# Kernel optimization log

Hardware: AMD Instinct MI355X
Metric: run time of the kernel (lower is better)

Reference implementation:

```python
import jax, jax.numpy as jnp
import numpy as np

B, N, L, K, CD, H, DH, D = 2, 2048, 1024, 16, 2, 4, 128, 128
HD = H * DH  # 512
FQ = 2.0  # embedding_freq_multiplier for query-invariant embedding
FV = 2.0  # embedding_freq_multiplier for value-invariant embedding
SCALE = 1.0 / float(np.sqrt(DH))


def _ln(x, s, b, eps=1e-6):
    m = x.mean(-1, keepdims=True)
    v = x.var(-1, keepdims=True)
    return (x - m) / jnp.sqrt(v + eps) * s + b


def _ffn(x, w1, b1, ls, lb, w2, b2):
    # PointwiseFFN: Dense -> gelu -> LayerNorm -> Dense
    h = jax.nn.gelu(x @ w1 + b1)
    return _ln(h, ls, lb) @ w2 + b2


def _rff(inv, Bm, freq, w1, b1, w2, b2):
    # random-Fourier-feature embedding of the invariant, then 2-layer MLP
    proj = (2.0 * jnp.pi * freq) * (inv @ Bm)          # (..., DH//2)
    feats = jnp.concatenate([jnp.sin(proj), jnp.cos(proj)], axis=-1)  # (..., DH)
    return jax.nn.gelu(feats @ w1 + b1) @ w2 + b2      # (..., DH)


def _forward(x, p, c, window_sigma, x_h,
             rffq, rffv,
             eq_w1, eq_b1, eq_w2, eq_b2,
             ev_w1, ev_b1, ev_w2, ev_b2,
             wq, bq, wk, bk, wv, bv,
             cw1, cb1, cls, clb, cw2, cb2,
             ivw1, ivb1, ivls, ivlb, ivw2, ivb2,
             mw1, mb1, mls, mlb, mw2, mb2,
             wo, bo):
    # relative-position invariant: (B, N, L, CD)
    rel = x[:, :, None, :] - p[:, None, :, :]
    dist = jnp.linalg.norm(rel, axis=-1)                         # (B, N, L)
    nearest = jnp.argsort(dist, axis=-1)[:, :, :K]               # (B, N, K)
    inv = jnp.take_along_axis(
        rel, jnp.broadcast_to(nearest[..., None], nearest.shape + (CD,)), axis=2)  # (B,N,K,CD)
    cg = jnp.take_along_axis(c[:, None, :, :], nearest[..., None], axis=2)         # (B,N,K,D)

    q = _rff(inv, rffq, FQ, eq_w1, eq_b1, eq_w2, eq_b2) @ wq + bq  # (B,N,K,HD)
    k_ = cg @ wk + bk                                              # (B,N,K,HD)
    v = cg @ wv + bv                                               # (B,N,K,HD)

    # conditioned value transform
    inv_emb_v = _rff(inv, rffv, FV, ev_w1, ev_b1, ev_w2, ev_b2)    # (B,N,K,DH)
    gb = _ffn(x_h, cw1, cb1, cls, clb, cw2, cb2)                   # (B,N,2*DH)
    g, bt = jnp.split(gb, 2, axis=-1)
    inv_emb_v = inv_emb_v * (1 + g[:, :, None, :]) + bt[:, :, None, :]
    vgb = _ffn(inv_emb_v, ivw1, ivb1, ivls, ivlb, ivw2, ivb2)      # (B,N,K,2*HD)
    vg, vb = jnp.split(vgb, 2, axis=-1)
    v = v * (1 + vg) + vb
    v = v.reshape(v.shape[:-1] + (H, DH))                          # (B,N,K,H,DH)
    v = _ffn(v, mw1, mb1, mls, mlb, mw2, mb2)

    q = q.reshape(q.shape[:-1] + (H, DH))
    k_ = k_.reshape(k_.shape[:-1] + (H, DH))
    att = (q * k_).sum(axis=-1) * SCALE                            # (B,N,K,H)

    # gaussian window in log-space, gathered at nearest latents
    gw_full = -0.5 * (dist ** 2)[..., None] / (window_sigma[:, None, :, :] ** 2)  # (B,N,L,1)
    gw = jnp.take_along_axis(gw_full, nearest[..., None], axis=2)                  # (B,N,K,1)
    att = jax.nn.softmax(att + gw, axis=-2)                        # softmax over K

    y = (att[..., None] * v).sum(axis=2)                           # (B,N,H,DH)
    y = y.reshape(y.shape[0], y.shape[1], HD)
    return y @ wo + bo                                             # (B,N,DH)


def setup_inputs() -> dict:
    key = jax.random.key(0)
    ks = jax.random.split(key, 24)
    dn = lambda k, i, o: jax.random.normal(k, (i, o), jnp.float32) / float(np.sqrt(i))
    z = lambda n: jnp.zeros((n,), jnp.float32)
    o = lambda n: jnp.ones((n,), jnp.float32)
    inp = {
        'x': jax.random.uniform(ks[0], (B, N, CD), jnp.float32),
        'p': jax.random.uniform(ks[1], (B, L, CD), jnp.float32),
        'c': jax.random.normal(ks[2], (B, L, D), jnp.float32),
        'window_sigma': jax.random.uniform(ks[3], (B, L, 1), jnp.float32, minval=0.1, maxval=0.5),
        'x_h': jax.random.normal(ks[4], (B, N, DH), jnp.float32),
        'rffq': jax.random.normal(ks[5], (CD, DH // 2), jnp.float32),
        'rffv': jax.random.normal(ks[6], (CD, DH // 2), jnp.float32),
        'eq_w1': dn(ks[7], DH, DH), 'eq_b1': z(DH),
        'eq_w2': dn(ks[8], DH, DH), 'eq_b2': z(DH),
        'ev_w1': dn(ks[9], DH, DH), 'ev_b1': z(DH),
        'ev_w2': dn(ks[10], DH, DH), 'ev_b2': z(DH),
        'wq': dn(ks[11], DH, HD), 'bq': z(HD),
        'wk': dn(ks[12], D, HD), 'bk': z(HD),
        'wv': dn(ks[13], D, HD), 'bv': z(HD),
        'cw1': dn(ks[14], DH, DH), 'cb1': z(DH), 'cls': o(DH), 'clb': z(DH),
        'cw2': dn(ks[15], DH, 2 * DH), 'cb2': z(2 * DH),
        'ivw1': dn(ks[16], DH, DH), 'ivb1': z(DH), 'ivls': o(DH), 'ivlb': z(DH),
        'ivw2': dn(ks[17], DH, 2 * HD), 'ivb2': z(2 * HD),
        'mw1': dn(ks[18], DH, DH), 'mb1': z(DH), 'mls': o(DH), 'mlb': z(DH),
        'mw2': dn(ks[19], DH, DH), 'mb2': z(DH),
        'wo': dn(ks[20], HD, DH), 'bo': z(DH),
    }
    return inp


def reference(x, p, c, window_sigma, x_h,
              rffq, rffv,
              eq_w1, eq_b1, eq_w2, eq_b2,
              ev_w1, ev_b1, ev_w2, ev_b2,
              wq, bq, wk, bk, wv, bv,
              cw1, cb1, cls, clb, cw2, cb2,
              ivw1, ivb1, ivls, ivlb, ivw2, ivb2,
              mw1, mb1, mls, mlb, mw2, mb2,
              wo, bo):
    return _forward(x, p, c, window_sigma, x_h,
                    rffq, rffv,
                    eq_w1, eq_b1, eq_w2, eq_b2,
                    ev_w1, ev_b1, ev_w2, ev_b2,
                    wq, bq, wk, bk, wv, bv,
                    cw1, cb1, cls, clb, cw2, cb2,
                    ivw1, ivb1, ivls, ivlb, ivw2, ivb2,
                    mw1, mb1, mls, mlb, mw2, mb2,
                    wo, bo)
```

## Files before the change

kernel.cpp:

```cpp
#include <hip/hip_runtime.h>
#include <hip/hip_bf16.h>
#include <math.h>

#define Bx  2
#define Nx  2048
#define Lx  1024
#define Kx  16
#define Hx  4
#define DHx 128
#define HDx 512
#define NROW 65536

typedef unsigned short u16;
typedef unsigned int   u32;
typedef unsigned long long u64;

#define ALD 132
#define KLD 520
#define LDW 136

typedef __attribute__((ext_vector_type(8))) short bf16x8;
typedef __attribute__((ext_vector_type(4))) float f32x4;
typedef __attribute__((ext_vector_type(4))) unsigned int u32x4;

__device__ __forceinline__ float bf(u16 v) { return __uint_as_float(((u32)v) << 16); }

__device__ __forceinline__ u16 f2bf(float f) {
  u32 u = __float_as_uint(f);
  u32 r = (u + 0x7fffu + ((u >> 16) & 1u)) >> 16;
  return (u16)r;
}

__device__ __forceinline__ void split2(float v, u16* h, u16* l) {
  u16 hh = f2bf(v);
  *h = hh;
  *l = f2bf(v - bf(hh));
}

__device__ __forceinline__ bf16x8 ntload8(const u16* p) {
  u32x4 v = __builtin_nontemporal_load((const u32x4*)p);
  bf16x8 r;
  *(u32x4*)&r = v;
  return r;
}

template <int ISB>
__device__ __forceinline__ float ldg1(const void* p, int i) {
  if (ISB) return bf(((const u16*)p)[i]);
  return ((const float*)p)[i];
}
template <int ISB>
__device__ __forceinline__ void ldg2(const void* p, int i, float& a, float& b) {
  if (ISB) {
    u32 u = *(const u32*)((const u16*)p + i);
    a = __uint_as_float(u << 16); b = __uint_as_float(u & 0xffff0000u);
  } else {
    float2 v = *(const float2*)((const float*)p + i);
    a = v.x; b = v.y;
  }
}
template <int ISB>
__device__ __forceinline__ void ldg4(const void* p, int i, float* o) {
  if (ISB) {
    uint2 u = *(const uint2*)((const u16*)p + i);
    o[0] = __uint_as_float(u.x << 16); o[1] = __uint_as_float(u.x & 0xffff0000u);
    o[2] = __uint_as_float(u.y << 16); o[3] = __uint_as_float(u.y & 0xffff0000u);
  } else {
    float4 v = *(const float4*)((const float*)p + i);
    o[0] = v.x; o[1] = v.y; o[2] = v.z; o[3] = v.w;
  }
}
template <int ISB>
__device__ __forceinline__ void ldg8(const void* p, int i, float* o) {
  if (ISB) {
    uint4 u = *(const uint4*)((const u16*)p + i);
    o[0] = __uint_as_float(u.x << 16); o[1] = __uint_as_float(u.x & 0xffff0000u);
// ... 495 lines not shown
    for (int r = 0; r < 16; r++) s += sm.ATT[r * 4 + h] * sm.KV[r * KLD + j];
    sm.YV[j] = s;
  }
  __syncthreads();

  if (t < 128) {
    float s = ldg1<ISB>(bo, t);
    for (int j = 0; j < 512; j++) s += sm.YV[j] * ldg1<ISB>(wo, j * 128 + t);
    stg1<ISB>(outp, bid * 128 + t, s);
  }
}


#define OFF_WQ    0
#define OFF_WK    65536
#define OFF_WV    131072
#define OFF_IVW2  196608
#define OFF_EQW1  327680
#define OFF_EQW2  344064
#define OFF_EVW1  360448
#define OFF_EVW2  376832
#define OFF_IVW1  393216
#define OFF_MW1   409600
#define OFF_MW2   425984
#define OFF_CW1   442368
#define OFF_CW2   458752
#define OFF_WO    491520
#define WT_TOTAL  557056

__device__ __attribute__((aligned(16))) u16 g_wth[WT_TOTAL];
__device__ __attribute__((aligned(16))) u16 g_wtl[WT_TOTAL];

__device__ __attribute__((aligned(16))) u16 gAh[NROW * 128], gAl[NROW * 128];
__device__ __attribute__((aligned(16))) u16 gBh[4096 * 128], gBl[4096 * 128];
__device__ __attribute__((aligned(16))) u16 gCGh[NROW * 128], gCGl[NROW * 128];
__device__ __attribute__((aligned(16))) u16 gVHh[NROW * 128], gVHl[NROW * 128];
__device__ __attribute__((aligned(16))) u16 gEIh[NROW * 128], gEIl[NROW * 128];
__device__ float gY[4096 * 512];
__device__ float gGVBT[4096 * 256];
__device__ float gATT[4096 * 64];
__device__ float gINVS[4096 * 32];
__device__ float gGWS[4096 * 16];
__device__ int   gIDX[NROW];

__global__ void k_prep32(
    const void* wq, const void* wk, const void* wv, const void* ivw2,
    const void* eqw1, const void* eqw2, const void* evw1, const void* evw2,
    const void* ivw1, const void* mw1, const void* mw2,
    const void* cw1, const void* cw2, const void* wo,
    const int* __restrict__ flag) {
  if (*flag != 0) return;
  int gid = blockIdx.x * 256 + threadIdx.x;
  float w;
  if (gid >= OFF_WO) {
    int local = gid - OFF_WO;
    int n = local >> 9, k = local & 511;
    w = ((const float*)wo)[k * 128 + n];
  } else {
    const float* src; int N; int local;
    if      (gid < OFF_WK)   { src = (const float*)wq;   N = 512;  local = gid - OFF_WQ; }
    else if (gid < OFF_WV)   { src = (const float*)wk;   N = 512;  local = gid - OFF_WK; }
    else if (gid < OFF_IVW2) { src = (const float*)wv;   N = 512;  local = gid - OFF_WV; }
    else if (gid < OFF_EQW1) { src = (const float*)ivw2; N = 1024; local = gid - OFF_IVW2; }
    else if (gid < OFF_EQW2) { src = (const float*)eqw1; N = 128;  local = gid - OFF_EQW1; }
    else if (gid < OFF_EVW1) { src = (const float*)eqw2; N = 128;  local = gid - OFF_EQW2; }
    else if (gid < OFF_EVW2) { src = (const float*)evw1; N = 128;  local = gid - OFF_EVW1; }
    else if (gid < OFF_IVW1) { src = (const float*)evw2; N = 128;  local = gid - OFF_EVW2; }
    else if (gid < OFF_MW1)  { src = (const float*)ivw1; N = 128;  local = gid - OFF_IVW1; }
    else if (gid < OFF_MW2)  { src = (const float*)mw1;  N = 128;  local = gid - OFF_MW1; }
    else if (gid < OFF_CW1)  { src = (const float*)mw2;  N = 128;  local = gid - OFF_MW2; }
    else if (gid < OFF_CW2)  { src = (const float*)cw1;  N = 128;  local = gid - OFF_CW1; }
    else                     { src = (const float*)cw2;  N = 256;  local = gid - OFF_CW2; }
    int n = local >> 7, k = local & 127;
    w = src[k * N + n];
  }
  u16 h = f2bf(w);
  g_wth[gid] = h;
  g_wtl[gid] = f2bf(w - bf(h));
}

__device__ __forceinline__ f32x4 mfma16(bf16x8 a, bf16x8 b, f32x4 c) {
  return __builtin_amdgcn_mfma_f32_16x16x32_bf16(a, b, c, 0, 0, 0);
}

__device__ __forceinline__ void stageW(
    const u16* __restrict__ wth, const u16* __restrict__ wtl, int srcStride,
    u16* __restrict__ sWh, u16* __restrict__ sWl, int t) {
#pragma unroll
  for (int it = 0; it < 4; it++) {
    int i = t + it * 512;
    int row = i >> 4, c8 = (i & 15) * 8;
    *(uint4*)(sWh + row * LDW + c8) = *(const uint4*)(wth + (size_t)row * srcStride + c8);
    *(uint4*)(sWl + row * LDW + c8) = *(const uint4*)(wtl + (size_t)row * srcStride + c8);
  }
}

__device__ __forceinline__ void loadA(
    const u16* __restrict__ Ah, const u16* __restrict__ Al, size_t abase,
    int lane, bf16x8 ah[4], bf16x8 al[4]) {
  int r = lane & 15, kg = lane >> 4;
#pragma unroll
  for (int kc = 0; kc < 4; kc++) {
    ah[kc] = *(const bf16x8*)(Ah + abase + (size_t)r * 128 + kc * 32 + kg * 8);
    al[kc] = *(const bf16x8*)(Al + abase + (size_t)r * 128 + kc * 32 + kg * 8);
  }
}

__device__ __forceinline__ void loadA_nt(
    const u16* __restrict__ Ah, const u16* __restrict__ Al, size_t abase,
    int lane, bf16x8 ah[4], bf16x8 al[4]) {
  int r = lane & 15, kg = lane >> 4;
#pragma unroll
  for (int kc = 0; kc < 4; kc++) {
    ah[kc] = ntload8(Ah + abase + (size_t)r * 128 + kc * 32 + kg * 8);
    al[kc] = ntload8(Al + abase + (size_t)r * 128 + kc * 32 + kg * 8);
  }
}

__device__ __forceinline__ void loadA_lds(
    const u16* __restrict__ sAh_w, const u16* __restrict__ sAl_w,
    int lane, bf16x8 ah[4], bf16x8 al[4]) {
  int r = lane & 15, kg = lane >> 4;
#pragma unroll
  for (int kc = 0; kc < 4; kc++) {
    ah[kc] = *(const bf16x8*)(sAh_w + r * LDW + kc * 32 + kg * 8);
    al[kc] = *(const bf16x8*)(sAl_w + r * LDW + kc * 32 + kg * 8);
  }
}

__device__ __forceinline__ void core16L(
    const bf16x8 ah[4], const bf16x8 al[4],
    const u16* __restrict__ sWh, const u16* __restrict__ sWl,
    f32x4 acc[8], int lane) {
  int r = lane & 15, kg = lane >> 4;
#pragma unroll
  for (int tile = 0; tile < 8; tile++) {
    int cc = tile * 16 + r;
    f32x4 a = {0.f, 0.f, 0.f, 0.f};
#pragma unroll
    for (int kc = 0; kc < 4; kc++) {
      bf16x8 bh = *(const bf16x8*)(sWh + cc * LDW + kc * 32 + kg * 8);
      bf16x8 bl = *(const bf16x8*)(sWl + cc * LDW + kc * 32 + kg * 8);
      a = mfma16(ah[kc], bh, a);
      a = mfma16(ah[kc], bl, a);
      a = mfma16(al[kc], bh, a);
    }
    acc[tile] = a;
  }
}

__device__ __forceinline__ void storeACT(
    f32x4 acc[8], const float* __restrict__ bias, int act,
    u16* __restrict__ sAh_w, u16* __restrict__ sAl_w, int lane) {
  int r = lane & 15, kg = lane >> 4;
#pragma unroll
  for (int tile = 0; tile < 8; tile++) {
    int cc = tile * 16 + r;
    float bc = bias[cc];
#pragma unroll
    for (int q = 0; q < 4; q++) {
      float v = acc[tile][q] + bc;
      if (act) v = geluf(v);
      int o = (kg * 4 + q) * LDW + cc;
      split2(v, sAh_w + o, sAl_w + o);
    }
  }
}

__device__ __forceinline__ void storeACT_ln(
    f32x4 acc[8], const float* __restrict__ bias,
    const float* __restrict__ sc, const float* __restrict__ bi,
    u16* __restrict__ sAh_w, u16* __restrict__ sAl_w, int lane) {
  int r = lane & 15, kg = lane >> 4;
  float v[8][4];
  float s[4] = {0.f, 0.f, 0.f, 0.f}, s2[4] = {0.f, 0.f, 0.f, 0.f};
#pragma unroll
  for (int tile = 0; tile < 8; tile++) {
    float bc = bias[tile * 16 + r];
#pragma unroll
    for (int q = 0; q < 4; q++) {
      float x = geluf(acc[tile][q] + bc);
      v[tile][q] = x; s[q] += x; s2[q] += x * x;
    }
  }
#pragma unroll
  for (int m = 1; m <= 8; m <<= 1) {
#pragma unroll
    for (int q = 0; q < 4; q++) {
      s[q]  += __shfl_xor(s[q], m);
      s2[q] += __shfl_xor(s2[q], m);
    }
  }
  float mean[4], rstd[4];
#pragma unroll
  for (int q = 0; q < 4; q++) {
// ... 55 lines not shown
    }
  }
}


__global__ __launch_bounds__(256) void k_topk(
    const float* __restrict__ x, const float* __restrict__ p,
    const float* __restrict__ sig, const int* __restrict__ flag) {
  if (*flag != 0) return;
  int t = threadIdx.x, lane = t & 63, w = t >> 6;
  int n = blockIdx.x * 4 + w, b = n >> 11;
  float qx = x[n * 2 + 0], qy = x[n * 2 + 1];
  u64 keys[16];
#pragma unroll
  for (int e = 0; e < 16; e++) {
    int l = e * 64 + lane;
    float px = p[(b * Lx + l) * 2 + 0];
    float py = p[(b * Lx + l) * 2 + 1];
    float dx = qx - px, dy = qy - py;
    float d2 = __fadd_rn(__fmul_rn(dx, dx), __fmul_rn(dy, dy));
    keys[e] = (((u64)__float_as_uint(__fsqrt_rn(d2))) << 32) | (u32)l;
  }
#pragma unroll 1
  for (int kk = 0; kk < Kx; kk++) {
    u64 kmin = keys[0];
#pragma unroll
    for (int e = 1; e < 16; e++) kmin = kmin < keys[e] ? kmin : keys[e];
#pragma unroll
    for (int m = 1; m <= 32; m <<= 1) {
      u64 o = shfl_xor_u64(kmin, m);
      kmin = kmin < o ? kmin : o;
    }
    if (lane == 0) {
      int l = (int)(kmin & 0xffffffffu);
      float d = __uint_as_float((u32)(kmin >> 32));
      float px = p[(b * Lx + l) * 2 + 0];
      float py = p[(b * Lx + l) * 2 + 1];
      float sg = sig[b * Lx + l];
      gIDX[n * 16 + kk] = l;
      gINVS[n * 32 + kk * 2 + 0] = qx - px;
      gINVS[n * 32 + kk * 2 + 1] = qy - py;
      gGWS[n * 16 + kk] = (-0.5f * (d * d)) / (sg * sg);
    }
#pragma unroll
    for (int e = 0; e < 16; e++) if (keys[e] == kmin) keys[e] = ~0ull;
  }
}

__global__ __launch_bounds__(512, 1) void k_c1(
    const float* __restrict__ xh, const float* __restrict__ cb1,
    const float* __restrict__ cls, const float* __restrict__ clb,
    const int* __restrict__ flag) {
  if (*flag != 0) return;
  __shared__ u16 sWh[128 * LDW], sWl[128 * LDW];
  int t = threadIdx.x, lane = t & 63, w = t >> 6;
  stageW(g_wth + OFF_CW1, g_wtl + OFF_CW1, 128, sWh, sWl, t);
  size_t rb = (size_t)blockIdx.x * 128 + w * 16;
  int r = lane & 15, kg = lane >> 4;
  bf16x8 ah[4], al[4];
#pragma unroll
  for (int kc = 0; kc < 4; kc++) {
    const float* src = xh + (rb + r) * 128 + kc * 32 + kg * 8;
#pragma unroll
    for (int e = 0; e < 8; e++) {
      float xv = src[e];
      u16 hh = f2bf(xv);
      ah[kc][e] = (short)hh;
      al[kc][e] = (short)f2bf(xv - bf(hh));
    }
  }
  __syncthreads();
  f32x4 acc[8];
  core16L(ah, al, sWh, sWl, acc, lane);
  store16_gelu_ln(acc, cb1, cls, clb, gBh, gBl, rb * 128, lane);
}

__global__ __launch_bounds__(512, 1) void k_c2(
    const float* __restrict__ cb2, const int* __restrict__ flag) {
  if (*flag != 0) return;
  __shared__ u16 sWh[128 * LDW], sWl[128 * LDW];
  int t = threadIdx.x, lane = t & 63, w = t >> 6;
  size_t rb = (size_t)blockIdx.x * 128 + w * 16;
  int r = lane & 15, kg = lane >> 4;
  bf16x8 ah[4], al[4];
  loadA(gBh, gBl, rb * 128, lane, ah, al);
#pragma unroll 1
  for (int half = 0; half < 2; half++) {
    stageW(g_wth + OFF_CW2 + half * 128 * 128,
           g_wtl + OFF_CW2 + half * 128 * 128, 128, sWh, sWl, t);
    __syncthreads();
    f32x4 acc[8];
    core16L(ah, al, sWh, sWl, acc, lane);
#pragma unroll
    for (int tile = 0; tile < 8; tile++) {
      int cc = half * 128 + tile * 16 + r;
      float bc = cb2[cc];
#pragma unroll
      for (int q = 0; q < 4; q++)
        gGVBT[(rb + kg * 4 + q) * 256 + cc] = acc[tile][q] + bc;
    }
    __syncthreads();
  }
}

__global__ __launch_bounds__(512) void k_gather(
    const float* __restrict__ c, const float* __restrict__ rffq,
    const float* __restrict__ rffv, const int* __restrict__ flag) {
  if (*flag != 0) return;
  int t = threadIdx.x;
  size_t row = (size_t)blockIdx.x * 64 + (t >> 3);
  int cbase = (t & 7) * 16;
  int n = (int)(row >> 4), b = n >> 11;
  int li = gIDX[row];
  const float* cp = c + ((size_t)(b * Lx + li)) * 128 + cbase;
  float ix = gINVS[n * 32 + (row & 15) * 2 + 0];
  float iy = gINVS[n * 32 + (row & 15) * 2 + 1];
  size_t o = row * 128 + cbase;
#pragma unroll
  for (int half = 0; half < 2; half++) {
    float4 va = ((const float4*)cp)[half * 2 + 0];
    float4 vb = ((const float4*)cp)[half * 2 + 1];
    float cv[8] = {va.x, va.y, va.z, va.w, vb.x, vb.y, vb.z, vb.w};
    bf16x8 ch_, cl_, qh_, ql_, eh_, el_;
#pragma unroll
    for (int j = 0; j < 8; j++) {
      int col = cbase + half * 8 + j, cc = col & 63;
      u16 hh = f2bf(cv[j]);
      ch_[j] = (short)hh; cl_[j] = (short)f2bf(cv[j] - bf(hh));
      float pq = 12.566370614359172f * (ix * rffq[cc] + iy * rffq[64 + cc]);
      float pv = 12.566370614359172f * (ix * rffv[cc] + iy * rffv[64 + cc]);
      float vq = (col < 64) ? sinf(pq) : cosf(pq);
      float vv = (col < 64) ? sinf(pv) : cosf(pv);
      u16 qh16 = f2bf(vq);
      qh_[j] = (short)qh16; ql_[j] = (short)f2bf(vq - bf(qh16));
      u16 eh16 = f2bf(vv);
      eh_[j] = (short)eh16; el_[j] = (short)f2bf(vv - bf(eh16));
    }
    *(bf16x8*)(gCGh + o + half * 8) = ch_;
    *(bf16x8*)(gCGl + o + half * 8) = cl_;
    *(bf16x8*)(gAh  + o + half * 8) = qh_;
    *(bf16x8*)(gAl  + o + half * 8) = ql_;
    *(bf16x8*)(gVHh + o + half * 8) = eh_;
    *(bf16x8*)(gVHl + o + half * 8) = el_;
  }
}

__global__ __launch_bounds__(512, 1) void k_qatt(
    const float* __restrict__ eqb1, const float* __restrict__ eqb2,
    const float* __restrict__ bq, const float* __restrict__ bk,
    const int* __restrict__ flag) {
  if (*flag != 0) return;
  __shared__ u16 sWh[128 * LDW], sWl[128 * LDW];
  __shared__ u16 sAh[128 * LDW], sAl[128 * LDW];
  int t = threadIdx.x, lane = t & 63, w = t >> 6;
  size_t rb = (size_t)blockIdx.x * 128 + w * 16;
  u16* myAh = sAh + (w * 16) * LDW;
  u16* myAl = sAl + (w * 16) * LDW;
  int r = lane & 15, kg = lane >> 4;
  stageW(g_wth + OFF_EQW1, g_wtl + OFF_EQW1, 128, sWh, sWl, t);
  bf16x8 ah[4], al[4];
  loadA_nt(gAh, gAl, rb * 128, lane, ah, al);
  __syncthreads();
  f32x4 acc[8];
  core16L(ah, al, sWh, sWl, acc, lane);
  storeACT(acc, eqb1, 1, myAh, myAl, lane);
  __syncthreads();
  stageW(g_wth + OFF_EQW2, g_wtl + OFF_EQW2, 128, sWh, sWl, t);
  __syncthreads();
  loadA_lds(myAh, myAl, lane, ah, al);
  core16L(ah, al, sWh, sWl, acc, lane);
  storeACT(acc, eqb2, 0, myAh, myAl, lane);
  bf16x8 qfh[4], qfl[4], ckh[4], ckl[4];
  loadA_lds(myAh, myAl, lane, qfh, qfl);
  loadA_nt(gCGh, gCGl, rb * 128, lane, ckh, ckl);
  int pt = blockIdx.x * 8 + w;
#pragma unroll 1
  for (int h = 0; h < 4; h++) {
    __syncthreads();
    stageW(g_wth + OFF_WQ + h * 16384, g_wtl + OFF_WQ + h * 16384, 128, sWh, sWl, t);
    __syncthreads();
    f32x4 dq[8];
    core16L(qfh, qfl, sWh, sWl, dq, lane);
    __syncthreads();
    stageW(g_wth + OFF_WK + h * 16384, g_wtl + OFF_WK + h * 16384, 128, sWh, sWl, t);
    __syncthreads();
    float pr[4] = {0.f, 0.f, 0.f, 0.f};
#pragma unroll
    for (int tile = 0; tile < 8; tile++) {
      int cc = tile * 16 + r;
      f32x4 dk = {0.f, 0.f, 0.f, 0.f};
#pragma unroll
      for (int kc = 0; kc < 4; kc++) {
        bf16x8 bh = *(const bf16x8*)(sWh + cc * LDW + kc * 32 + kg * 8);
        bf16x8 bl = *(const bf16x8*)(sWl + cc * LDW + kc * 32 + kg * 8);
        dk = mfma16(ckh[kc], bh, dk);
        dk = mfma16(ckh[kc], bl, dk);
        dk = mfma16(ckl[kc], bh, dk);
      }
      float bqv = bq[h * 128 + cc], bkv = bk[h * 128 + cc];
#pragma unroll
      for (int q = 0; q < 4; q++)
        pr[q] += (dq[tile][q] + bqv) * (dk[q] + bkv);
    }
#pragma unroll
    for (int m = 1; m <= 8; m <<= 1) {
#pragma unroll
      for (int q = 0; q < 4; q++) pr[q] += __shfl_xor(pr[q], m);
    }
    if (r == 0) {
#pragma unroll
      for (int q = 0; q < 4; q++)
        gATT[pt * 64 + h * 16 + kg * 4 + q] = pr[q] * 0.08838834764831845f;
    }
  }
}

__global__ __launch_bounds__(256) void k_soft(const int* __restrict__ flag) {
  if (*flag != 0) return;
  int id = blockIdx.x * 256 + threadIdx.x;
  int pt = id >> 2, h = id & 3;
  float mx = -1e30f;
  for (int k = 0; k < 16; k++) {
    float v = gATT[pt * 64 + h * 16 + k] + gGWS[pt * 16 + k];
    mx = fmaxf(mx, v);
  }
  float ssum = 0.0f;
  float ev[16];
  for (int k = 0; k < 16; k++) {
    float e = expf(gATT[pt * 64 + h * 16 + k] + gGWS[pt * 16 + k] - mx);
    ev[k] = e; ssum += e;
  }
  float inv = 1.0f / fmaxf(ssum, 1e-37f);
  for (int k = 0; k < 16; k++) gATT[pt * 64 + h * 16 + k] = ev[k] * inv;
}

__global__ __launch_bounds__(512, 1) void k_echain(
    const float* __restrict__ evb1, const float* __restrict__ evb2,
    const float* __restrict__ ivb1, const float* __restrict__ ivls,
    const float* __restrict__ ivlb, const int* __restrict__ flag) {
  if (*flag != 0) return;
  __shared__ u16 sWh[128 * LDW], sWl[128 * LDW];
  __shared__ u16 sAh[128 * LDW], sAl[128 * LDW];
  int t = threadIdx.x, lane = t & 63, w = t >> 6;
  size_t rb = (size_t)blockIdx.x * 128 + w * 16;
  u16* myAh = sAh + (w * 16) * LDW;
  u16* myAl = sAl + (w * 16) * LDW;
  int r = lane & 15, kg = lane >> 4;
  int pt = blockIdx.x * 8 + w;
  stageW(g_wth + OFF_EVW1, g_wtl + OFF_EVW1, 128, sWh, sWl, t);
  bf16x8 ah[4], al[4];
  loadA_nt(gVHh, gVHl, rb * 128, lane, ah, al);
  __syncthreads();
  f32x4 acc[8];
  core16L(ah, al, sWh, sWl, acc, lane);
  storeACT(acc, evb1, 1, myAh, myAl, lane);
  __syncthreads();
  stageW(g_wth + OFF_EVW2, g_wtl + OFF_EVW2, 128, sWh, sWl, t);
  __syncthreads();
  loadA_lds(myAh, myAl, lane, ah, al);
  core16L(ah, al, sWh, sWl, acc, lane);
#pragma unroll
  for (int tile = 0; tile < 8; tile++) {
    int cc = tile * 16 + r;
    float bc = evb2[cc];
    float gv = gGVBT[pt * 256 + cc];
    float bt = gGVBT[pt * 256 + 128 + cc];
#pragma unroll
    for (int q = 0; q < 4; q++) {
      float v = (acc[tile][q] + bc) * (1.0f + gv) + bt;
      int o = (kg * 4 + q) * LDW + cc;
      split2(v, myAh + o, myAl + o);
    }
  }
  __syncthreads();
  stageW(g_wth + OFF_IVW1, g_wtl + OFF_IVW1, 128, sWh, sWl, t);
  __syncthreads();
  loadA_lds(myAh, myAl, lane, ah, al);
  core16L(ah, al, sWh, sWl, acc, lane);
  store16_gelu_ln(acc, ivb1, ivls, ivlb, gEIh, gEIl, rb * 128, lane);
}

__global__ __launch_bounds__(512, 1) void k_vchain(
    const float* __restrict__ bv, const float* __restrict__ ivb2,
    const float* __restrict__ mb1, const float* __restrict__ mls,
    const float* __restrict__ mlb, const float* __restrict__ mb2,
    const int* __restrict__ flag) {
  if (*flag != 0) return;
  __shared__ u16 sWh[128 * LDW], sWl[128 * LDW];
  __shared__ u16 sAh[128 * LDW], sAl[128 * LDW];
  int t = threadIdx.x, lane = t & 63, w = t >> 6;
  size_t rb = (size_t)blockIdx.x * 128 + w * 16;
  u16* myAh = sAh + (w * 16) * LDW;
  u16* myAl = sAl + (w * 16) * LDW;
  int r = lane & 15, kg = lane >> 4;
  int pt = blockIdx.x * 8 + w;
#pragma unroll 1
  for (int h = 0; h < 4; h++) {
    f32x4 vv[8];
    __syncthreads();
    stageW(g_wth + OFF_WV + (size_t)(h * 128) * 128,
           g_wtl + OFF_WV + (size_t)(h * 128) * 128, 128, sWh, sWl, t);
    {
      bf16x8 ckh[4], ckl[4];
      loadA_nt(gCGh, gCGl, rb * 128, lane, ckh, ckl);
      __syncthreads();
      core16L(ckh, ckl, sWh, sWl, vv, lane);
    }
    f32x4 ag[8];
    __syncthreads();
    stageW(g_wth + OFF_IVW2 + (size_t)(h * 128) * 128,
           g_wtl + OFF_IVW2 + (size_t)(h * 128) * 128, 128, sWh, sWl, t);
    {
      bf16x8 eih[4], eil[4];
      loadA_nt(gEIh, gEIl, rb * 128, lane, eih, eil);
      __syncthreads();
      core16L(eih, eil, sWh, sWl, ag, lane);
    }
    __syncthreads();
    stageW(g_wth + OFF_IVW2 + (size_t)(512 + h * 128) * 128,
           g_wtl + OFF_IVW2 + (size_t)(512 + h * 128) * 128, 128, sWh, sWl, t);
    {
      bf16x8 eih[4], eil[4];
      loadA_nt(gEIh, gEIl, rb * 128, lane, eih, eil);
      __syncthreads();
#pragma unroll
      for (int tile = 0; tile < 8; tile++) {
        int cc = tile * 16 + r;
        f32x4 ab = {0.f, 0.f, 0.f, 0.f};
#pragma unroll
        for (int kc = 0; kc < 4; kc++) {
          bf16x8 bh = *(const bf16x8*)(sWh + cc * LDW + kc * 32 + kg * 8);
          bf16x8 bl = *(const bf16x8*)(sWl + cc * LDW + kc * 32 + kg * 8);
          ab = mfma16(eih[kc], bh, ab);
          ab = mfma16(eih[kc], bl, ab);
          ab = mfma16(eil[kc], bh, ab);
        }
        float bvv = bv[h * 128 + cc];
        float bgv = ivb2[h * 128 + cc], bbv = ivb2[512 + h * 128 + cc];
#pragma unroll
        for (int q = 0; q < 4; q++) {
          float x = vv[tile][q] + bvv;
          u16 hh = f2bf(x);
          u16 ll = f2bf(x - bf(hh));
          float v = bf(hh) + bf(ll);
          float nv = v * (1.f + (ag[tile][q] + bgv)) + (ab[q] + bbv);
          int o = (kg * 4 + q) * LDW + cc;
          split2(nv, myAh + o, myAl + o);
        }
      }
    }
    __syncthreads();
    stageW(g_wth + OFF_MW1, g_wtl + OFF_MW1, 128, sWh, sWl, t);
    __syncthreads();
    {
      bf16x8 vh_[4], vl_[4];
      loadA_lds(myAh, myAl, lane, vh_, vl_);
      f32x4 acc[8];
      core16L(vh_, vl_, sWh, sWl, acc, lane);
      storeACT_ln(acc, mb1, mls, mlb, myAh, myAl, lane);
    }
    __syncthreads();
    stageW(g_wth + OFF_MW2, g_wtl + OFF_MW2, 128, sWh, sWl, t);
    __syncthreads();
    {
      bf16x8 vh_[4], vl_[4];
      loadA_lds(myAh, myAl, lane, vh_, vl_);
      f32x4 acc[8];
      core16L(vh_, vl_, sWh, sWl, acc, lane);
      float attv[4];
#pragma unroll
      for (int q = 0; q < 4; q++) attv[q] = gATT[pt * 64 + h * 16 + kg * 4 + q];
#pragma unroll
      for (int tile = 0; tile < 8; tile++) {
        int cc = tile * 16 + r;
        float mb = mb2[cc];
        float s = 0.f;
#pragma unroll
        for (int q = 0; q < 4; q++) s += attv[q] * (acc[tile][q] + mb);
        s += __shfl_xor(s, 16);
        s += __shfl_xor(s, 32);
        if (kg == 0) gY[(size_t)pt * 512 + h * 128 + cc] = s;
      }
    }
  }
}

__global__ __launch_bounds__(512, 1) void k_out(
    const float* __restrict__ bo, const int* __restrict__ flag,
    float* __restrict__ outp) {
  if (*flag != 0) return;
  __shared__ u16 sWh[128 * LDW], sWl[128 * LDW];
  int t = threadIdx.x, lane = t & 63, w = t >> 6;
  size_t rb = (size_t)blockIdx.x * 128 + w * 16;
  int r = lane & 15, kg = lane >> 4;
  f32x4 acc[8] = {};
#pragma unroll 1
  for (int kb = 0; kb < 4; kb++) {
    stageW(g_wth + OFF_WO + kb * 128, g_wtl + OFF_WO + kb * 128, 512, sWh, sWl, t);
    bf16x8 ah[4], al[4];
#pragma unroll
    for (int kc = 0; kc < 4; kc++) {
      const float* src = gY + (rb + r) * 512 + kb * 128 + kc * 32 + kg * 8;
#pragma unroll
      for (int e = 0; e < 8; e++) {
        float xv = src[e];
        u16 hh = f2bf(xv);
        ah[kc][e] = (short)hh;
        al[kc][e] = (short)f2bf(xv - bf(hh));
      }
    }
    __syncthreads();
#pragma unroll
    for (int tile = 0; tile < 8; tile++) {
      int cc = tile * 16 + r;
      f32x4 a = acc[tile];
#pragma unroll
      for (int kc = 0; kc < 4; kc++) {
        bf16x8 bh = *(const bf16x8*)(sWh + cc * LDW + kc * 32 + kg * 8);
        bf16x8 bl = *(const bf16x8*)(sWl + cc * LDW + kc * 32 + kg * 8);
        a = mfma16(ah[kc], bh, a);
        a = mfma16(ah[kc], bl, a);
        a = mfma16(al[kc], bh, a);
      }
      acc[tile] = a;
    }
    __syncthreads();
  }
#pragma unroll
  for (int tile = 0; tile < 8; tile++) {
    int cc = tile * 16 + r;
    float bc = bo[cc];
#pragma unroll
    for (int q = 0; q < 4; q++)
      outp[(rb + kg * 4 + q) * 128 + cc] = acc[tile][q] + bc;
  }
}

extern "C" void kernel_launch(void* const* d_in, const int* in_sizes, int n_in,
                              void* d_out, int out_size, void* d_ws, size_t ws_size,
                              hipStream_t stream) {
  (void)in_sizes; (void)n_in; (void)out_size; (void)ws_size;
  int* flag = (int*)d_ws;

  k_sniff<<<1, 64, 0, stream>>>(d_in[23], flag);

  k_prep32<<<WT_TOTAL / 256, 256, 0, stream>>>(
      d_in[15], d_in[17], d_in[19], d_in[31],
      d_in[7], d_in[9], d_in[11], d_in[13],
      d_in[27], d_in[33], d_in[37],
      d_in[21], d_in[25], d_in[39], flag);

  k_topk<<<1024, 256, 0, stream>>>((const float*)d_in[0], (const float*)d_in[1],
                                   (const float*)d_in[3], flag);
  k_c1<<<32, 512, 0, stream>>>((const float*)d_in[4], (const float*)d_in[22],
                               (const float*)d_in[23], (const float*)d_in[24], flag);
  k_c2<<<32, 512, 0, stream>>>((const float*)d_in[26], flag);
  k_gather<<<1024, 512, 0, stream>>>((const float*)d_in[2], (const float*)d_in[5],
                                     (const float*)d_in[6], flag);
  k_qatt<<<512, 512, 0, stream>>>((const float*)d_in[8], (const float*)d_in[10],
                                  (const float*)d_in[16], (const float*)d_in[18], flag);
  k_soft<<<64, 256, 0, stream>>>(flag);
  k_echain<<<512, 512, 0, stream>>>((const float*)d_in[12], (const float*)d_in[14],
                                    (const float*)d_in[28], (const float*)d_in[29],
                                    (const float*)d_in[30], flag);
  k_vchain<<<512, 512, 0, stream>>>((const float*)d_in[20], (const float*)d_in[32],
                                    (const float*)d_in[34], (const float*)d_in[35],
                                    (const float*)d_in[36], (const float*)d_in[38], flag);
  k_out<<<32, 512, 0, stream>>>((const float*)d_in[40], flag, (float*)d_out);

  k_fused<1><<<Bx * Nx, 256, 0, stream>>>(
      d_in[0], d_in[1], d_in[2], d_in[3], d_in[4], d_in[5], d_in[6],
      d_in[7], d_in[8], d_in[9], d_in[10],
// ... 8 lines not shown
```

Before: 732.0 us.

## Stage weights via global_load_lds DMA with XOR-swizzled layout and half-tile overlap

Weights are pre-swizzled in the prep kernel with an XOR pattern so they can be copied into unpadded 128x128 LDS tiles with direct global-to-LDS loads instead of register round-trips. Each weight tile is staged in two halves so the second half's load overlaps MFMA work on the first, and several redundant barriers are dropped. The intent is to cut LDS staging latency and bank conflicts. It relies on careful barrier placement around async LDS writes, which risks races if the ordering is wrong.

Result: slower. 781.7 us (+6.8%).

```diff
diff --git a/kernel.cpp b/kernel.cpp
--- a/kernel.cpp
+++ b/kernel.cpp
@@ -22,6 +22,9 @@
 typedef __attribute__((ext_vector_type(8))) short bf16x8;
 typedef __attribute__((ext_vector_type(4))) float f32x4;
 typedef __attribute__((ext_vector_type(4))) unsigned int u32x4;
+
+typedef const __attribute__((address_space(1))) void* as1_cvp;
+typedef __attribute__((address_space(3))) void* as3_vp;
 
 __device__ __forceinline__ float bf(u16 v) { return __uint_as_float(((u32)v) << 16); }
 
@@ -623,46 +626,75 @@
   if (*flag != 0) return;
   int gid = blockIdx.x * 256 + threadIdx.x;
   float w;
+  int dest;
   if (gid >= OFF_WO) {
     int local = gid - OFF_WO;
     int n = local >> 9, k = local & 511;
     w = ((const float*)wo)[k * 128 + n];
+    int cs = ((k >> 3) & 15) ^ (n & 15);
+    dest = OFF_WO + n * 512 + (k & 384) + (cs << 3) + (k & 7);
   } else {
-    const float* src; int N; int local;
-    if      (gid < OFF_WK)   { src = (const float*)wq;   N = 512;  local = gid - OFF_WQ; }
-    else if (gid < OFF_WV)   { src = (const float*)wk;   N = 512;  local = gid - OFF_WK; }
-    else if (gid < OFF_IVW2) { src = (const float*)wv;   N = 512;  local = gid - OFF_WV; }
-    else if (gid < OFF_EQW1) { src = (const float*)ivw2; N = 1024; local = gid - OFF_IVW2; }
-    else if (gid < OFF_EQW2) { src = (const float*)eqw1; N = 128;  local = gid - OFF_EQW1; }
-    else if (gid < OFF_EVW1) { src = (const float*)eqw2; N = 128;  local = gid - OFF_EQW2; }
-    else if (gid < OFF_EVW2) { src = (const float*)evw1; N = 128;  local = gid - OFF_EVW1; }
-    else if (gid < OFF_IVW1) { src = (const float*)evw2; N = 128;  local = gid - OFF_EVW2; }
-    else if (gid < OFF_MW1)  { src = (const float*)ivw1; N = 128;  local = gid - OFF_IVW1; }
-    else if (gid < OFF_MW2)  { src = (const float*)mw1;  N = 128;  local = gid - OFF_MW1; }
-    else if (gid < OFF_CW1)  { src = (const float*)mw2;  N = 128;  local = gid - OFF_MW2; }
-    else if (gid < OFF_CW2)  { src = (const float*)cw1;  N = 128;  local = gid - OFF_CW1; }
-    else                     { src = (const float*)cw2;  N = 256;  local = gid - OFF_CW2; }
+    const float* src; int N; int local; int base;
+    if      (gid < OFF_WK)   { src = (const float*)wq;   N = 512;  local = gid - OFF_WQ;   base = OFF_WQ; }
+    else if (gid < OFF_WV)   { src = (const float*)wk;   N = 512;  local = gid - OFF_WK;   base = OFF_WK; }
+    else if (gid < OFF_IVW2) { src = (const float*)wv;   N = 512;  local = gid - OFF_WV;   base = OFF_WV; }
+    else if (gid < OFF_EQW1) { src = (const float*)ivw2; N = 1024; local = gid - OFF_IVW2; base = OFF_IVW2; }
+    else if (gid < OFF_EQW2) { src = (const float*)eqw1; N = 128;  local = gid - OFF_EQW1; base = OFF_EQW1; }
+    else if (gid < OFF_EVW1) { src = (const float*)eqw2; N = 128;  local = gid - OFF_EQW2; base = OFF_EQW2; }
+    else if (gid < OFF_EVW2) { src = (const float*)evw1; N = 128;  local = gid - OFF_EVW1; base = OFF_EVW1; }
+    else if (gid < OFF_IVW1) { src = (const float*)evw2; N = 128;  local = gid - OFF_EVW2; base = OFF_EVW2; }
+    else if (gid < OFF_MW1)  { src = (const float*)ivw1; N = 128;  local = gid - OFF_IVW1; base = OFF_IVW1; }
+    else if (gid < OFF_MW2)  { src = (const float*)mw1;  N = 128;  local = gid - OFF_MW1;  base = OFF_MW1; }
+    else if (gid < OFF_CW1)  { src = (const float*)mw2;  N = 128;  local = gid - OFF_MW2;  base = OFF_MW2; }
+    else if (gid < OFF_CW2)  { src = (const float*)cw1;  N = 128;  local = gid - OFF_CW1;  base = OFF_CW1; }
+    else                     { src = (const float*)cw2;  N = 256;  local = gid - OFF_CW2;  base = OFF_CW2; }
     int n = local >> 7, k = local & 127;
     w = src[k * N + n];
+    int cs = (k >> 3) ^ (n & 15);
+    dest = base + n * 128 + (cs << 3) + (k & 7);
   }
   u16 h = f2bf(w);
-  g_wth[gid] = h;
-  g_wtl[gid] = f2bf(w - bf(h));
+  g_wth[dest] = h;
+  g_wtl[dest] = f2bf(w - bf(h));
 }
 
 __device__ __forceinline__ f32x4 mfma16(bf16x8 a, bf16x8 b, f32x4 c) {
   return __builtin_amdgcn_mfma_f32_16x16x32_bf16(a, b, c, 0, 0, 0);
 }
 
-__device__ __forceinline__ void stageW(
+__device__ __forceinline__ const bf16x8* wp(const u16* sW, int cc, int kc, int kg) {
+  return (const bf16x8*)(sW + cc * 128 + (((kc * 4 + kg) ^ (cc & 15)) << 3));
+}
+
+__device__ __forceinline__ void gll16(const u16* g, u16* l) {
+  __builtin_amdgcn_global_load_lds((as1_cvp)(const void*)g, (as3_vp)(void*)l, 16, 0, 0);
+}
+
+__device__ __forceinline__ void stageDMA(
     const u16* __restrict__ wth, const u16* __restrict__ wtl, int srcStride,
-    u16* __restrict__ sWh, u16* __restrict__ sWl, int t) {
+    u16* sWh, u16* sWl, int t) {
+  int w6 = t >> 6, lane = t & 63;
 #pragma unroll
   for (int it = 0; it < 4; it++) {
-    int i = t + it * 512;
-    int row = i >> 4, c8 = (i & 15) * 8;
-    *(uint4*)(sWh + row * LDW + c8) = *(const uint4*)(wth + (size_t)row * srcStride + c8);
-    *(uint4*)(sWl + row * LDW + c8) = *(const uint4*)(wtl + (size_t)row * srcStride + c8);
+    int seg = it * 8 + w6;
+    int chunk = seg * 64 + lane;
+    int row = chunk >> 4, cs = chunk & 15;
+    gll16(wth + (size_t)row * srcStride + cs * 8, sWh + (size_t)seg * 512);
+    gll16(wtl + (size_t)row * srcStride + cs * 8, sWl + (size_t)seg * 512);
+  }
+}
+
+__device__ __forceinline__ void stageH(
+    const u16* __restrict__ wth, const u16* __restrict__ wtl,
+    u16* sWh, u16* sWl, int t, int half) {
+  int w6 = t >> 6, lane = t & 63;
+#pragma unroll
+  for (int it = 0; it < 2; it++) {
+    int seg = half * 16 + it * 8 + w6;
+    int chunk = seg * 64 + lane;
+    int row = chunk >> 4, cs = chunk & 15;
+    gll16(wth + (size_t)row * 128 + cs * 8, sWh + (size_t)seg * 512);
+    gll16(wtl + (size_t)row * 128 + cs * 8, sWl + (size_t)seg * 512);
   }
 }
 
@@ -699,19 +731,20 @@
   }
 }
 
-__device__ __forceinline__ void core16L(
+template <int T0, int T1>
+__device__ __forceinline__ void core16L_r(
     const bf16x8 ah[4], const bf16x8 al[4],
     const u16* __restrict__ sWh, const u16* __restrict__ sWl,
     f32x4 acc[8], int lane) {
   int r = lane & 15, kg = lane >> 4;
 #pragma unroll
-  for (int tile = 0; tile < 8; tile++) {
+  for (int tile = T0; tile < T1; tile++) {
     int cc = tile * 16 + r;
     f32x4 a = {0.f, 0.f, 0.f, 0.f};
 #pragma unroll
     for (int kc = 0; kc < 4; kc++) {
-      bf16x8 bh = *(const bf16x8*)(sWh + cc * LDW + kc * 32 + kg * 8);
-      bf16x8 bl = *(const bf16x8*)(sWl + cc * LDW + kc * 32 + kg * 8);
+      bf16x8 bh = *wp(sWh, cc, kc, kg);
+      bf16x8 bl = *wp(sWl, cc, kc, kg);
       a = mfma16(ah[kc], bh, a);
       a = mfma16(ah[kc], bl, a);
       a = mfma16(al[kc], bh, a);
@@ -873,9 +906,9 @@
     const float* __restrict__ cls, const float* __restrict__ clb,
     const int* __restrict__ flag) {
   if (*flag != 0) return;
-  __shared__ u16 sWh[128 * LDW], sWl[128 * LDW];
+  __shared__ u16 sWh[128 * 128], sWl[128 * 128];
   int t = threadIdx.x, lane = t & 63, w = t >> 6;
-  stageW(g_wth + OFF_CW1, g_wtl + OFF_CW1, 128, sWh, sWl, t);
+  stageDMA(g_wth + OFF_CW1, g_wtl + OFF_CW1, 128, sWh, sWl, t);
   size_t rb = (size_t)blockIdx.x * 128 + w * 16;
   int r = lane & 15, kg = lane >> 4;
   bf16x8 ah[4], al[4];
@@ -892,14 +925,14 @@
   }
   __syncthreads();
   f32x4 acc[8];
-  core16L(ah, al, sWh, sWl, acc, lane);
+  core16L_r<0, 8>(ah, al, sWh, sWl, acc, lane);
   store16_gelu_ln(acc, cb1, cls, clb, gBh, gBl, rb * 128, lane);
 }
 
 __global__ __launch_bounds__(512, 1) void k_c2(
     const float* __restrict__ cb2, const int* __restrict__ flag) {
   if (*flag != 0) return;
-  __shared__ u16 sWh[128 * LDW], sWl[128 * LDW];
+  __shared__ u16 sWh[128 * 128], sWl[128 * 128];
   int t = threadIdx.x, lane = t & 63, w = t >> 6;
   size_t rb = (size_t)blockIdx.x * 128 + w * 16;
   int r = lane & 15, kg = lane >> 4;
@@ -907,11 +940,11 @@
   loadA(gBh, gBl, rb * 128, lane, ah, al);
 #pragma unroll 1
   for (int half = 0; half < 2; half++) {
-    stageW(g_wth + OFF_CW2 + half * 128 * 128,
-           g_wtl + OFF_CW2 + half * 128 * 128, 128, sWh, sWl, t);
+    stageDMA(g_wth + OFF_CW2 + half * 128 * 128,
+             g_wtl + OFF_CW2 + half * 128 * 128, 128, sWh, sWl, t);
     __syncthreads();
     f32x4 acc[8];
-    core16L(ah, al, sWh, sWl, acc, lane);
+    core16L_r<0, 8>(ah, al, sWh, sWl, acc, lane);
 #pragma unroll
     for (int tile = 0; tile < 8; tile++) {
       int cc = half * 128 + tile * 16 + r;
@@ -971,25 +1004,30 @@
     const float* __restrict__ bq, const float* __restrict__ bk,
     const int* __restrict__ flag) {
   if (*flag != 0) return;
-  __shared__ u16 sWh[128 * LDW], sWl[128 * LDW];
+  __shared__ u16 sWh[128 * 128], sWl[128 * 128];
   __shared__ u16 sAh[128 * LDW], sAl[128 * LDW];
   int t = threadIdx.x, lane = t & 63, w = t >> 6;
   size_t rb = (size_t)blockIdx.x * 128 + w * 16;
   u16* myAh = sAh + (w * 16) * LDW;
   u16* myAl = sAl + (w * 16) * LDW;
   int r = lane & 15, kg = lane >> 4;
-  stageW(g_wth + OFF_EQW1, g_wtl + OFF_EQW1, 128, sWh, sWl, t);
+  stageH(g_wth + OFF_EQW1, g_wtl + OFF_EQW1, sWh, sWl, t, 0);
   bf16x8 ah[4], al[4];
   loadA_nt(gAh, gAl, rb * 128, lane, ah, al);
   __syncthreads();
+  stageH(g_wth + OFF_EQW1, g_wtl + OFF_EQW1, sWh, sWl, t, 1);
   f32x4 acc[8];
-  core16L(ah, al, sWh, sWl, acc, lane);
+  core16L_r<0, 4>(ah, al, sWh, sWl, acc, lane);
+  __syncthreads();
+  core16L_r<4, 8>(ah, al, sWh, sWl, acc, lane);
   storeACT(acc, eqb1, 1, myAh, myAl, lane);
-  __syncthreads();
-  stageW(g_wth + OFF_EQW2, g_wtl + OFF_EQW2, 128, sWh, sWl, t);
-  __syncthreads();
+  stageH(g_wth + OFF_EQW2, g_wtl + OFF_EQW2, sWh, sWl, t, 0);
+  __syncthreads();
+  stageH(g_wth + OFF_EQW2, g_wtl + OFF_EQW2, sWh, sWl, t, 1);
   loadA_lds(myAh, myAl, lane, ah, al);
-  core16L(ah, al, sWh, sWl, acc, lane);
+  core16L_r<0, 4>(ah, al, sWh, sWl, acc, lane);
+  __syncthreads();
+  core16L_r<4, 8>(ah, al, sWh, sWl, acc, lane);
   storeACT(acc, eqb2, 0, myAh, myAl, lane);
   bf16x8 qfh[4], qfl[4], ckh[4], ckl[4];
   loadA_lds(myAh, myAl, lane, qfh, qfl);
@@ -997,31 +1035,55 @@
   int pt = blockIdx.x * 8 + w;
 #pragma unroll 1
   for (int h = 0; h < 4; h++) {
-    __syncthreads();
-    stageW(g_wth + OFF_WQ + h * 16384, g_wtl + OFF_WQ + h * 16384, 128, sWh, sWl, t);
-    __syncthreads();
+    stageH(g_wth + OFF_WQ + h * 16384, g_wtl + OFF_WQ + h * 16384, sWh, sWl, t, 0);
+    __syncthreads();
+    stageH(g_wth + OFF_WQ + h * 16384, g_wtl + OFF_WQ + h * 16384, sWh, sWl, t, 1);
     f32x4 dq[8];
-    core16L(qfh, qfl, sWh, sWl, dq, lane);
-    __syncthreads();
-    stageW(g_wth + OFF_WK + h * 16384, g_wtl + OFF_WK + h * 16384, 128, sWh, sWl, t);
-    __syncthreads();
+    core16L_r<0, 4>(qfh, qfl, sWh, sWl, dq, lane);
+    __syncthreads();
+    core16L_r<4, 8>(qfh, qfl, sWh, sWl, dq, lane);
+    stageH(g_wth + OFF_WK + h * 16384, g_wtl + OFF_WK + h * 16384, sWh, sWl, t, 0);
+    float bqv[8], bkv[8];
+#pragma unroll
+    for (int tile = 0; tile < 8; tile++) {
+      bqv[tile] = bq[h * 128 + tile * 16 + r];
+      bkv[tile] = bk[h * 128 + tile * 16 + r];
+    }
+    __syncthreads();
+    stageH(g_wth + OFF_WK + h * 16384, g_wtl + OFF_WK + h * 16384, sWh, sWl, t, 1);
     float pr[4] = {0.f, 0.f, 0.f, 0.f};
 #pragma unroll
-    for (int tile = 0; tile < 8; tile++) {
+    for (int tile = 0; tile < 4; tile++) {
       int cc = tile * 16 + r;
       f32x4 dk = {0.f, 0.f, 0.f, 0.f};
 #pragma unroll
       for (int kc = 0; kc < 4; kc++) {
-        bf16x8 bh = *(const bf16x8*)(sWh + cc * LDW + kc * 32 + kg * 8);
-        bf16x8 bl = *(const bf16x8*)(sWl + cc * LDW + kc * 32 + kg * 8);
+        bf16x8 bh = *wp(sWh, cc, kc, kg);
+        bf16x8 bl = *wp(sWl, cc, kc, kg);
         dk = mfma16(ckh[kc], bh, dk);
         dk = mfma16(ckh[kc], bl, dk);
         dk = mfma16(ckl[kc], bh, dk);
       }
-      float bqv = bq[h * 128 + cc], bkv = bk[h * 128 + cc];
 #pragma unroll
       for (int q = 0; q < 4; q++)
-        pr[q] += (dq[tile][q] + bqv) * (dk[q] + bkv);
+        pr[q] += (dq[tile][q] + bqv[tile]) * (dk[q] + bkv[tile]);
+    }
+    __syncthreads();
+#pragma unroll
+    for (int tile = 4; tile < 8; tile++) {
+      int cc = tile * 16 + r;
+      f32x4 dk = {0.f, 0.f, 0.f, 0.f};
+#pragma unroll
+      for (int kc = 0; kc < 4; kc++) {
+        bf16x8 bh = *wp(sWh, cc, kc, kg);
+        bf16x8 bl = *wp(sWl, cc, kc, kg);
+        dk = mfma16(ckh[kc], bh, dk);
+        dk = mfma16(ckh[kc], bl, dk);
+        dk = mfma16(ckl[kc], bh, dk);
+      }
+#pragma unroll
+      for (int q = 0; q < 4; q++)
+        pr[q] += (dq[tile][q] + bqv[tile]) * (dk[q] + bkv[tile]);
     }
 #pragma unroll
     for (int m = 1; m <= 8; m <<= 1) {
@@ -1060,7 +1122,7 @@
     const float* __restrict__ ivb1, const float* __restrict__ ivls,
     const float* __restrict__ ivlb, const int* __restrict__ flag) {
   if (*flag != 0) return;
-  __shared__ u16 sWh[128 * LDW], sWl[128 * LDW];
+  __shared__ u16 sWh[128 * 128], sWl[128 * 128];
   __shared__ u16 sAh[128 * LDW], sAl[128 * LDW];
   int t = threadIdx.x, lane = t & 63, w = t >> 6;
   size_t rb = (size_t)blockIdx.x * 128 + w * 16;
@@ -1068,18 +1130,23 @@
   u16* myAl = sAl + (w * 16) * LDW;
   int r = lane & 15, kg = lane >> 4;
   int pt = blockIdx.x * 8 + w;
-  stageW(g_wth + OFF_EVW1, g_wtl + OFF_EVW1, 128, sWh, sWl, t);
+  stageH(g_wth + OFF_EVW1, g_wtl + OFF_EVW1, sWh, sWl, t, 0);
   bf16x8 ah[4], al[4];
   loadA_nt(gVHh, gVHl, rb * 128, lane, ah, al);
   __syncthreads();
+  stageH(g_wth + OFF_EVW1, g_wtl + OFF_EVW1, sWh, sWl, t, 1);
   f32x4 acc[8];
-  core16L(ah, al, sWh, sWl, acc, lane);
+  core16L_r<0, 4>(ah, al, sWh, sWl, acc, lane);
+  __syncthreads();
+  core16L_r<4, 8>(ah, al, sWh, sWl, acc, lane);
   storeACT(acc, evb1, 1, myAh, myAl, lane);
-  __syncthreads();
-  stageW(g_wth + OFF_EVW2, g_wtl + OFF_EVW2, 128, sWh, sWl, t);
-  __syncthreads();
+  stageH(g_wth + OFF_EVW2, g_wtl + OFF_EVW2, sWh, sWl, t, 0);
+  __syncthreads();
+  stageH(g_wth + OFF_EVW2, g_wtl + OFF_EVW2, sWh, sWl, t, 1);
   loadA_lds(myAh, myAl, lane, ah, al);
-  core16L(ah, al, sWh, sWl, acc, lane);
+  core16L_r<0, 4>(ah, al, sWh, sWl, acc, lane);
+  __syncthreads();
+  core16L_r<4, 8>(ah, al, sWh, sWl, acc, lane);
 #pragma unroll
   for (int tile = 0; tile < 8; tile++) {
     int cc = tile * 16 + r;
@@ -1093,11 +1160,13 @@
       split2(v, myAh + o, myAl + o);
     }
   }
-  __syncthreads();
-  stageW(g_wth + OFF_IVW1, g_wtl + OFF_IVW1, 128, sWh, sWl, t);
-  __syncthreads();
+  stageH(g_wth + OFF_IVW1, g_wtl + OFF_IVW1, sWh, sWl, t, 0);
+  __syncthreads();
+  stageH(g_wth + OFF_IVW1, g_wtl + OFF_IVW1, sWh, sWl, t, 1);
   loadA_lds(myAh, myAl, lane, ah, al);
-  core16L(ah, al, sWh, sWl, acc, lane);
+  core16L_r<0, 4>(ah, al, sWh, sWl, acc, lane);
+  __syncthreads();
+  core16L_r<4, 8>(ah, al, sWh, sWl, acc, lane);
   store16_gelu_ln(acc, ivb1, ivls, ivlb, gEIh, gEIl, rb * 128, lane);
 }
 
@@ -1107,7 +1176,7 @@
     const float* __restrict__ mlb, const float* __restrict__ mb2,
     const int* __restrict__ flag) {
   if (*flag != 0) return;
-  __shared__ u16 sWh[128 * LDW], sWl[128 * LDW];
+  __shared__ u16 sWh[128 * 128], sWl[128 * 128];
   __shared__ u16 sAh[128 * LDW], sAl[128 * LDW];
   int t = threadIdx.x, lane = t & 63, w = t >> 6;
   size_t rb = (size_t)blockIdx.x * 128 + w * 16;
@@ -1118,40 +1187,48 @@
 #pragma unroll 1
   for (int h = 0; h < 4; h++) {
     f32x4 vv[8];
-    __syncthreads();
-    stageW(g_wth + OFF_WV + (size_t)(h * 128) * 128,
-           g_wtl + OFF_WV + (size_t)(h * 128) * 128, 128, sWh, sWl, t);
+    stageH(g_wth + OFF_WV + (size_t)h * 16384,
+           g_wtl + OFF_WV + (size_t)h * 16384, sWh, sWl, t, 0);
     {
       bf16x8 ckh[4], ckl[4];
       loadA_nt(gCGh, gCGl, rb * 128, lane, ckh, ckl);
       __syncthreads();
-      core16L(ckh, ckl, sWh, sWl, vv, lane);
+      stageH(g_wth + OFF_WV + (size_t)h * 16384,
+             g_wtl + OFF_WV + (size_t)h * 16384, sWh, sWl, t, 1);
+      core16L_r<0, 4>(ckh, ckl, sWh, sWl, vv, lane);
+      __syncthreads();
+      core16L_r<4, 8>(ckh, ckl, sWh, sWl, vv, lane);
     }
     f32x4 ag[8];
-    __syncthreads();
-    stageW(g_wth + OFF_IVW2 + (size_t)(h * 128) * 128,
-           g_wtl + OFF_IVW2 + (size_t)(h * 128) * 128, 128, sWh, sWl, t);
+    stageH(g_wth + OFF_IVW2 + (size_t)h * 16384,
+           g_wtl + OFF_IVW2 + (size_t)h * 16384, sWh, sWl, t, 0);
     {
       bf16x8 eih[4], eil[4];
       loadA_nt(gEIh, gEIl, rb * 128, lane, eih, eil);
       __syncthreads();
-      core16L(eih, eil, sWh, sWl, ag, lane);
-    }
-    __syncthreads();
-    stageW(g_wth + OFF_IVW2 + (size_t)(512 + h * 128) * 128,
-           g_wtl + OFF_IVW2 + (size_t)(512 + h * 128) * 128, 128, sWh, sWl, t);
+      stageH(g_wth + OFF_IVW2 + (size_t)h * 16384,
+             g_wtl + OFF_IVW2 + (size_t)h * 16384, sWh, sWl, t, 1);
+      core16L_r<0, 4>(eih, eil, sWh, sWl, ag, lane);
+      __syncthreads();
+      core16L_r<4, 8>(eih, eil, sWh, sWl, ag, lane);
+    }
+    stageH(g_wth + OFF_IVW2 + (size_t)(512 + h * 128) * 128,
+           g_wtl + OFF_IVW2 + (size_t)(512 + h * 128) * 128, sWh, sWl, t, 0);
     {
       bf16x8 eih[4], eil[4];
       loadA_nt(gEIh, gEIl, rb * 128, lane, eih, eil);
       __syncthreads();
+      stageH(g_wth + OFF_IVW2 + (size_t)(512 + h * 128) * 128,
+             g_wtl + OFF_IVW2 + (size_t)(512 + h * 128) * 128, sWh, sWl, t, 1);
+      __syncthreads();
 #pragma unroll
       for (int tile = 0; tile < 8; tile++) {
         int cc = tile * 16 + r;
         f32x4 ab = {0.f, 0.f, 0.f, 0.f};
 #pragma unroll
         for (int kc = 0; kc < 4; kc++) {
-          bf16x8 bh = *(const bf16x8*)(sWh + cc * LDW + kc * 32 + kg * 8);
-          bf16x8 bl = *(const bf16x8*)(sWl + cc * LDW + kc * 32 + kg * 8);
+          bf16x8 bh = *wp(sWh, cc, kc, kg);
+          bf16x8 bl = *wp(sWl, cc, kc, kg);
           ab = mfma16(eih[kc], bh, ab);
           ab = mfma16(eih[kc], bl, ab);
           ab = mfma16(eil[kc], bh, ab);
@@ -1171,23 +1248,28 @@
       }
     }
     __syncthreads();
-    stageW(g_wth + OFF_MW1, g_wtl + OFF_MW1, 128, sWh, sWl, t);
-    __syncthreads();
+    stageH(g_wth + OFF_MW1, g_wtl + OFF_MW1, sWh, sWl, t, 0);
+    __syncthreads();
+    stageH(g_wth + OFF_MW1, g_wtl + OFF_MW1, sWh, sWl, t, 1);
     {
       bf16x8 vh_[4], vl_[4];
       loadA_lds(myAh, myAl, lane, vh_, vl_);
       f32x4 acc[8];
-      core16L(vh_, vl_, sWh, sWl, acc, lane);
+      core16L_r<0, 4>(vh_, vl_, sWh, sWl, acc, lane);
+      __syncthreads();
+      core16L_r<4, 8>(vh_, vl_, sWh, sWl, acc, lane);
       storeACT_ln(acc, mb1, mls, mlb, myAh, myAl, lane);
     }
-    __syncthreads();
-    stageW(g_wth + OFF_MW2, g_wtl + OFF_MW2, 128, sWh, sWl, t);
-    __syncthreads();
+    stageH(g_wth + OFF_MW2, g_wtl + OFF_MW2, sWh, sWl, t, 0);
+    __syncthreads();
+    stageH(g_wth + OFF_MW2, g_wtl + OFF_MW2, sWh, sWl, t, 1);
     {
       bf16x8 vh_[4], vl_[4];
       loadA_lds(myAh, myAl, lane, vh_, vl_);
       f32x4 acc[8];
-      core16L(vh_, vl_, sWh, sWl, acc, lane);
+      core16L_r<0, 4>(vh_, vl_, sWh, sWl, acc, lane);
+      __syncthreads();
+      core16L_r<4, 8>(vh_, vl_, sWh, sWl, acc, lane);
       float attv[4];
 #pragma unroll
       for (int q = 0; q < 4; q++) attv[q] = gATT[pt * 64 + h * 16 + kg * 4 + q];
@@ -1210,14 +1292,14 @@
     const float* __restrict__ bo, const int* __restrict__ flag,
     float* __restrict__ outp) {
   if (*flag != 0) return;
-  __shared__ u16 sWh[128 * LDW], sWl[128 * LDW];
+  __shared__ u16 sWh[128 * 128], sWl[128 * 128];
   int t = threadIdx.x, lane = t & 63, w = t >> 6;
   size_t rb = (size_t)blockIdx.x * 128 + w * 16;
   int r = lane & 15, kg = lane >> 4;
   f32x4 acc[8] = {};
 #pragma unroll 1
   for (int kb = 0; kb < 4; kb++) {
-    stageW(g_wth + OFF_WO + kb * 128, g_wtl + OFF_WO + kb * 128, 512, sWh, sWl, t);
+    stageDMA(g_wth + OFF_WO + kb * 128, g_wtl + OFF_WO + kb * 128, 512, sWh, sWl, t);
     bf16x8 ah[4], al[4];
 #pragma unroll
     for (int kc = 0; kc < 4; kc++) {
@@ -1237,8 +1319,8 @@
       f32x4 a = acc[tile];
 #pragma unroll
       for (int kc = 0; kc < 4; kc++) {
-        bf16x8 bh = *(const bf16x8*)(sWh + cc * LDW + kc * 32 + kg * 8);
-        bf16x8 bl = *(const bf16x8*)(sWl + cc * LDW + kc * 32 + kg * 8);
+        bf16x8 bh = *wp(sWh, cc, kc, kg);
+        bf16x8 bl = *wp(sWl, cc, kc, kg);
         a = mfma16(ah[kc], bh, a);
         a = mfma16(ah[kc], bl, a);
         a = mfma16(al[kc], bh, a);
```
